# Kernel optimization log

Measured on AMD Instinct MI355X. Metric: run time of the kernel, lower is better.

Reference implementation:

```python
import jax, jax.numpy as jnp
import numpy as np

IN_BIT = 8      # in_bit_width
W_BIT = 2       # weight_bit_width (also output act quantizer bit width)
BN_EPS = 1e-4


def _ste(x, q):
    # straight-through estimator: forward = q, backward = identity w.r.t. x
    return x + jax.lax.stop_gradient(q - x)


def act_quant(x, bit):
    # CommonActQuant: signed int quant, narrow_range=False, power-of-two scale
    # range [-1, 1 - 2^{-(bit-1)}] -> scale = 2^{-(bit-1)}
    s = 2.0 ** (1 - bit)
    n_min = -(2.0 ** (bit - 1))
    n_max = 2.0 ** (bit - 1) - 1.0
    q = jnp.clip(jnp.round(x / s), n_min, n_max) * s
    return _ste(x, q)


def weight_quant(w, bit):
    # CommonWeightQuant: narrow-range signed int quant, unit scaling const
    # scale = 1 / (2^{bit-1} - 1); for bit=2 levels are {-1, 0, 1}
    n = 2.0 ** (bit - 1) - 1.0
    s = 1.0 / n
    q = jnp.clip(jnp.round(w / s), -n, n) * s
    return _ste(w, q)


def setup_inputs() -> dict:
    key = jax.random.key(0)
    k1, k2, k3, k4 = jax.random.split(key, 4)
    B, C, H, W = 32, 256, 32, 32
    x = jax.random.normal(k1, (B, C, H, W), dtype=jnp.float32) * 0.5
    weight = jax.random.normal(k2, (C, C, 3, 3), dtype=jnp.float32) * 0.5
    gamma = jnp.ones((C,), dtype=jnp.float32)
    beta = jnp.zeros((C,), dtype=jnp.float32)
    running_mean = jax.random.normal(k3, (C,), dtype=jnp.float32) * 0.1
    running_var = jax.random.uniform(k4, (C,), dtype=jnp.float32, minval=0.5, maxval=1.5)
    return {"x": x, "weight": weight, "gamma": gamma, "beta": beta,
            "running_mean": running_mean, "running_var": running_var}


def reference(x, weight, gamma, beta, running_mean, running_var):
    # 1) input QuantIdentity (8-bit, [-1, 1-2^-7], power-of-two scale 2^-7)
    xq = act_quant(x, IN_BIT)
    # 2) QuantConv2d 3x3 stride 1 pad 1, no bias, 2-bit weights
    wq = weight_quant(weight, W_BIT)
    y = jax.lax.conv_general_dilated(
        xq, wq, window_strides=(1, 1), padding=((1, 1), (1, 1)),
        dimension_numbers=("NCHW", "OIHW", "NCHW"))
    # 3) BatchNorm2d (inference, eps=1e-4)
    inv = gamma / jnp.sqrt(running_var + BN_EPS)
    y = y * inv[None, :, None, None] + (beta - running_mean * inv)[None, :, None, None]
    # 4) output QuantIdentity at weight_bit_width bits
    return act_quant(y, W_BIT)
```

## Files before the change

### kernel.cpp

```cpp
#include <hip/hip_runtime.h>
#include <hip/hip_bf16.h>
#include <stdint.h>


typedef int i32x4 __attribute__((ext_vector_type(4)));
typedef float f32x4 __attribute__((ext_vector_type(4)));

__device__ __forceinline__ void gload_lds16(const void* g, const void* lds) {
    __builtin_amdgcn_global_load_lds(
        (const __attribute__((address_space(1))) unsigned int*)(uintptr_t)g,
        (__attribute__((address_space(3))) unsigned int*)(uintptr_t)lds,
        16, 0, 0);
}

__global__ __launch_bounds__(256) void quant_kernel(
    const float* __restrict__ x, const float* __restrict__ w,
    signed char* __restrict__ xpad, signed char* __restrict__ wq)
{
    __shared__ signed char tile[32 * 272];
    const int t = threadIdx.x;
    const int blk = blockIdx.x;

    if (blk >= 1088) {
        const int co = blk - 1088;
        signed char* wt = tile;
#pragma unroll
        for (int p = 0; p < 9; ++p) {
            const int idx = p * 256 + t;
            const float v = w[co * 2304 + idx];
            const int ci = idx / 9;
            const int khkw = idx - 9 * ci;
            const float q = fminf(fmaxf(rintf(v), -1.f), 1.f);
            wt[khkw * 256 + ci] = (signed char)(int)q;
        }
        __syncthreads();
        if (t < 144) {
            const int kt = t >> 2, kq = t & 3;
            const uint4 v = *(const uint4*)(wt + t * 16);
            *(uint4*)(wq + ((size_t)((co >> 4) * 36 + kt) << 10) + kq * 256 + (co & 15) * 16) = v;
        }
        return;
    }

    const int b = blk / 34;
    const int hp = blk % 34;
    signed char* rowbase = xpad + (size_t)((b * 34 + hp) * 34) * 256;
    const uint4 z = {0u, 0u, 0u, 0u};
    if (hp == 0 || hp == 33) {
        for (int i = t; i < 544; i += 256) *(uint4*)(rowbase + i * 16) = z;
        return;
    }
    const int h = hp - 1;
    const int ww = t & 31;
    const int cg = (t >> 5) * 4;
#pragma unroll
    for (int p = 0; p < 8; ++p) {
        const int ci = p * 32 + cg;
        unsigned packed = 0;
#pragma unroll
        for (int k = 0; k < 4; ++k) {
            const float v = x[(((size_t)(b * 256 + ci + k)) * 32 + h) * 32 + ww];
            float q = fminf(fmaxf(rintf(__fmul_rn(v, 128.f)), -128.f), 127.f);
            packed |= ((unsigned)(unsigned char)(signed char)(int)q) << (8 * k);
        }
        *(unsigned*)(tile + ww * 272 + ci) = packed;
    }
    __syncthreads();
#pragma unroll
    for (int q = 0; q < 2; ++q) {
        const int wp = q * 16 + (t >> 4);
        const int ci16 = (t & 15) * 16;
        uint4 v = *(const uint4*)(tile + wp * 272 + ci16);
        *(uint4*)(rowbase + (size_t)(wp + 1) * 256 + ci16) = v;
    }
    if (t < 32) {
        const int wp = (t >> 4) * 33;
        *(uint4*)(rowbase + (size_t)wp * 256 + (t & 15) * 16) = z;
    }
}

__global__ __launch_bounds__(256, 3) void conv_gemm_kernel(
    const signed char* __restrict__ xpad, const signed char* __restrict__ wqm,
    const float* __restrict__ gamma, const float* __restrict__ beta,
    const float* __restrict__ mean, const float* __restrict__ var,
    float* __restrict__ out)
{
    __shared__ signed char As[6 * 34 * 256];

    const int tid = threadIdx.x;
    const int wv = tid >> 6;
    const int lane = tid & 63;
    const int l16 = lane & 15;
    const int l4 = lane >> 4;

    const int mt = blockIdx.x >> 1;
    const int n0 = (blockIdx.x & 1) * 128;
    const int b = mt >> 3;
    const int h0 = (mt & 7) * 4;
    const int wave_m = wv & 1;
    const int wave_n = wv >> 1;

    const signed char* xbase = xpad + (size_t)(b * 34 + h0) * 34 * 256;
#pragma unroll
    for (int p = 0; p < 13; ++p) {
        const int i = p * 4 + wv;
        if (i < 51) {
            const int d = i * 64 + lane;
            const int r = d >> 4;
            const int c = d & 15;
            gload_lds16(xbase + r * 256 + ((c ^ (r & 15)) << 4), As + i * 1024);
        }
    }
    __syncthreads();

    int r0[4];
#pragma unroll
    for (int i = 0; i < 4; ++i)
        r0[i] = (wave_m * 2 + (i >> 1)) * 34 + (i & 1) * 16 + l16;

    const signed char* bp[4];
#pragma unroll
    for (int j = 0; j < 4; ++j)
        bp[j] = wqm + (((size_t)((n0 >> 4) + wave_n * 4 + j) * 36) << 10) + lane * 16;

    i32x4 acc[4][4];
#pragma unroll
    for (int i = 0; i < 4; i++)
#pragma unroll
        for (int j = 0; j < 4; j++) acc[i][j] = (i32x4){0, 0, 0, 0};

    i32x4 aP[2][4], bP[2][4];

#define LOAD_B(kt, dst) { _Pragma("unroll") \
                          for (int j = 0; j < 4; ++j) \
                              dst[j] = *(const i32x4*)(bp[j] + (kt) * 1024); }
#define LOAD_A(kt, dst) { const int khkw = (kt) >> 2; \
                          const int kh = khkw / 3; \
                          const int kw = khkw - 3 * kh; \
                          const int roff = kh * 34 + kw; \
                          const int cb = ((kt) & 3) * 4 + l4; \
                          _Pragma("unroll") \
                          for (int i = 0; i < 4; ++i) { \
                              const int r = r0[i] + roff; \
                              dst[i] = *(const i32x4*)(As + r * 256 + ((cb ^ (r & 15)) << 4)); \
                          } }
#define MFMA(af, bf) { _Pragma("unroll") \
                       for (int i = 0; i < 4; ++i) \
                           _Pragma("unroll") \
                           for (int j = 0; j < 4; ++j) \
                               acc[i][j] = __builtin_amdgcn_mfma_i32_16x16x64_i8(af[i], bf[j], acc[i][j], 0, 0, 0); }

    LOAD_B(0, bP[0])
    LOAD_A(0, aP[0])
#pragma unroll
    for (int kt = 0; kt < 36; ++kt) {
        const int cur = kt & 1, nxt = cur ^ 1;
        if (kt + 1 < 36) { LOAD_B(kt + 1, bP[nxt]) LOAD_A(kt + 1, aP[nxt]) }
        MFMA(aP[cur], bP[cur])
    }

#pragma unroll
    for (int j = 0; j < 4; ++j) {
        const int co = n0 + wave_n * 64 + j * 16 + l16;
        const float iv = __fdiv_rn(gamma[co], __fsqrt_rn(__fadd_rn(var[co], 1e-4f)));
        const float bias = __fsub_rn(beta[co], __fmul_rn(mean[co], iv));
#pragma unroll
        for (int i = 0; i < 4; ++i) {
            const int h = h0 + wave_m * 2 + (i >> 1);
            const int w = (i & 1) * 16 + l4 * 4;
            f32x4 v;
#pragma unroll
            for (int r = 0; r < 4; r++) {
                const float y = __fmul_rn((float)acc[i][j][r], 0.0078125f);
                const float t = __fadd_rn(__fmul_rn(y, iv), bias);
                float z = rintf(__fmul_rn(t, 2.f));
                z = fminf(fmaxf(z, -2.f), 1.f);
                v[r] = __fmul_rn(z, 0.5f);
            }
            *(f32x4*)(&out[(((size_t)(b * 256 + co)) * 32 + h) * 32 + w]) = v;
        }
    }
#undef LOAD_B
#undef LOAD_A
#undef MFMA
}

extern "C" void kernel_launch(void* const* d_in, const int* in_sizes, int n_in,
                              void* d_out, int out_size, void* d_ws, size_t ws_size,
                              hipStream_t stream) {
    const float* x      = (const float*)d_in[0];
    const float* weight = (const float*)d_in[1];
    const float* gamma  = (const float*)d_in[2];
    const float* beta   = (const float*)d_in[3];
    const float* rmean  = (const float*)d_in[4];
    const float* rvar   = (const float*)d_in[5];
    float* out = (float*)d_out;

    signed char* wq   = (signed char*)d_ws;
    signed char* xpad = (signed char*)d_ws + (1 << 20);

    quant_kernel<<<1344, 256, 0, stream>>>(x, weight, xpad, wq);
    conv_gemm_kernel<<<512, 256, 0, stream>>>(xpad, wq, gamma, beta, rmean, rvar, out);
}
```

Before: 127.4 us.

## Pack ternary weights as 4-bit nibbles and double waves per conv block

Weights are stored offset by one as 4-bit values, two nibbles per byte, which halves the global bytes read for the B operand. They are expanded back to int8 in registers with a byte-permute lookup before each MFMA. The conv block grows from 4 to 8 waves, each handling one output row instead of two, so per-wave accumulators are halved and more waves share the LDS input tile. The cost is extra VALU unpack work per MFMA and a changed launch configuration.

```diff
diff --git a/kernel.cpp b/kernel.cpp
--- a/kernel.cpp
+++ b/kernel.cpp
@@ -31,13 +31,17 @@
             const int ci = idx / 9;
             const int khkw = idx - 9 * ci;
             const float q = fminf(fmaxf(rintf(v), -1.f), 1.f);
-            wt[khkw * 256 + ci] = (signed char)(int)q;
+            wt[khkw * 256 + ci] = (signed char)(int)(q + 1.f);
         }
         __syncthreads();
         if (t < 144) {
             const int kt = t >> 2, kq = t & 3;
             const uint4 v = *(const uint4*)(wt + t * 16);
-            *(uint4*)(wq + ((size_t)((co >> 4) * 36 + kt) << 10) + kq * 256 + (co & 15) * 16) = v;
+            uint2 o;
+            o.x = v.x | (v.y << 4);
+            o.y = v.z | (v.w << 4);
+            *(uint2*)(wq + ((size_t)((co >> 4) * 18 + (kt >> 1)) << 10)
+                         + ((kq * 16 + (co & 15)) << 4) + (kt & 1) * 8) = o;
         }
         return;
     }
@@ -79,7 +83,7 @@
     }
 }
 
-__global__ __launch_bounds__(256, 3) void conv_gemm_kernel(
+__global__ __launch_bounds__(512, 4) void conv_gemm_kernel(
     const signed char* __restrict__ xpad, const signed char* __restrict__ wqm,
     const float* __restrict__ gamma, const float* __restrict__ beta,
     const float* __restrict__ mean, const float* __restrict__ var,
@@ -97,13 +101,13 @@
     const int n0 = (blockIdx.x & 1) * 128;
     const int b = mt >> 3;
     const int h0 = (mt & 7) * 4;
-    const int wave_m = wv & 1;
-    const int wave_n = wv >> 1;
+    const int wave_m = wv & 3;
+    const int wave_n = wv >> 2;
 
     const signed char* xbase = xpad + (size_t)(b * 34 + h0) * 34 * 256;
 #pragma unroll
-    for (int p = 0; p < 13; ++p) {
-        const int i = p * 4 + wv;
+    for (int p = 0; p < 7; ++p) {
+        const int i = p * 8 + wv;
         if (i < 51) {
             const int d = i * 64 + lane;
             const int r = d >> 4;
@@ -113,50 +117,64 @@
     }
     __syncthreads();
 
-    int r0[4];
-#pragma unroll
-    for (int i = 0; i < 4; ++i)
-        r0[i] = (wave_m * 2 + (i >> 1)) * 34 + (i & 1) * 16 + l16;
-
-    const signed char* bp[4];
+    int r0[2];
+#pragma unroll
+    for (int i = 0; i < 2; ++i)
+        r0[i] = wave_m * 34 + i * 16 + l16;
+
+    const signed char* pbp[4];
 #pragma unroll
     for (int j = 0; j < 4; ++j)
-        bp[j] = wqm + (((size_t)((n0 >> 4) + wave_n * 4 + j) * 36) << 10) + lane * 16;
-
-    i32x4 acc[4][4];
-#pragma unroll
-    for (int i = 0; i < 4; i++)
+        pbp[j] = wqm + (((size_t)(((n0 >> 4) + wave_n * 4 + j) * 18)) << 10) + lane * 16;
+
+    i32x4 acc[2][4];
+#pragma unroll
+    for (int i = 0; i < 2; i++)
 #pragma unroll
         for (int j = 0; j < 4; j++) acc[i][j] = (i32x4){0, 0, 0, 0};
 
-    i32x4 aP[2][4], bP[2][4];
-
-#define LOAD_B(kt, dst) { _Pragma("unroll") \
-                          for (int j = 0; j < 4; ++j) \
-                              dst[j] = *(const i32x4*)(bp[j] + (kt) * 1024); }
+    i32x4 aP[2][2];
+    i32x4 pB[2][4];
+
+    const unsigned LUTC = 0x000100FFu;
+    const unsigned NMSK = 0x0F0F0F0Fu;
+
+#define LOAD_PB(kt2, dst) { _Pragma("unroll") \
+                            for (int j = 0; j < 4; ++j) \
+                                dst[j] = *(const i32x4*)(pbp[j] + (kt2) * 1024); }
 #define LOAD_A(kt, dst) { const int khkw = (kt) >> 2; \
                           const int kh = khkw / 3; \
                           const int kw = khkw - 3 * kh; \
                           const int roff = kh * 34 + kw; \
                           const int cb = ((kt) & 3) * 4 + l4; \
                           _Pragma("unroll") \
-                          for (int i = 0; i < 4; ++i) { \
+                          for (int i = 0; i < 2; ++i) { \
                               const int r = r0[i] + roff; \
                               dst[i] = *(const i32x4*)(As + r * 256 + ((cb ^ (r & 15)) << 4)); \
                           } }
-#define MFMA(af, bf) { _Pragma("unroll") \
-                       for (int i = 0; i < 4; ++i) \
-                           _Pragma("unroll") \
-                           for (int j = 0; j < 4; ++j) \
-                               acc[i][j] = __builtin_amdgcn_mfma_i32_16x16x64_i8(af[i], bf[j], acc[i][j], 0, 0, 0); }
-
-    LOAD_B(0, bP[0])
+#define COMPUTE(af, src, half) { _Pragma("unroll") \
+    for (int j = 0; j < 4; ++j) { \
+        const unsigned d0 = (unsigned)src[j][(half) * 2]; \
+        const unsigned d1 = (unsigned)src[j][(half) * 2 + 1]; \
+        i32x4 bU; \
+        bU[0] = (int)__builtin_amdgcn_perm(0u, LUTC, d0 & NMSK); \
+        bU[1] = (int)__builtin_amdgcn_perm(0u, LUTC, (d0 >> 4) & NMSK); \
+        bU[2] = (int)__builtin_amdgcn_perm(0u, LUTC, d1 & NMSK); \
+        bU[3] = (int)__builtin_amdgcn_perm(0u, LUTC, (d1 >> 4) & NMSK); \
+        acc[0][j] = __builtin_amdgcn_mfma_i32_16x16x64_i8(af[0], bU, acc[0][j], 0, 0, 0); \
+        acc[1][j] = __builtin_amdgcn_mfma_i32_16x16x64_i8(af[1], bU, acc[1][j], 0, 0, 0); \
+    } }
+
+    LOAD_PB(0, pB[0])
     LOAD_A(0, aP[0])
 #pragma unroll
     for (int kt = 0; kt < 36; ++kt) {
         const int cur = kt & 1, nxt = cur ^ 1;
-        if (kt + 1 < 36) { LOAD_B(kt + 1, bP[nxt]) LOAD_A(kt + 1, aP[nxt]) }
-        MFMA(aP[cur], bP[cur])
+        const int kt2 = kt >> 1;
+        const int pcur = kt2 & 1, pnxt = pcur ^ 1;
+        if ((kt & 1) == 0 && kt2 + 1 < 18) { LOAD_PB(kt2 + 1, pB[pnxt]) }
+        if (kt + 1 < 36) { LOAD_A(kt + 1, aP[nxt]) }
+        COMPUTE(aP[cur], pB[pcur], kt & 1)
     }
 
 #pragma unroll
@@ -164,10 +182,10 @@
         const int co = n0 + wave_n * 64 + j * 16 + l16;
         const float iv = __fdiv_rn(gamma[co], __fsqrt_rn(__fadd_rn(var[co], 1e-4f)));
         const float bias = __fsub_rn(beta[co], __fmul_rn(mean[co], iv));
-#pragma unroll
-        for (int i = 0; i < 4; ++i) {
-            const int h = h0 + wave_m * 2 + (i >> 1);
-            const int w = (i & 1) * 16 + l4 * 4;
+        const int h = h0 + wave_m;
+#pragma unroll
+        for (int i = 0; i < 2; ++i) {
+            const int w = i * 16 + l4 * 4;
             f32x4 v;
 #pragma unroll
             for (int r = 0; r < 4; r++) {
@@ -180,9 +198,9 @@
             *(f32x4*)(&out[(((size_t)(b * 256 + co)) * 32 + h) * 32 + w]) = v;
         }
     }
-#undef LOAD_B
+#undef LOAD_PB
 #undef LOAD_A
-#undef MFMA
+#undef COMPUTE
 }
 
 extern "C" void kernel_launch(void* const* d_in, const int* in_sizes, int n_in,
@@ -200,5 +218,5 @@
     signed char* xpad = (signed char*)d_ws + (1 << 20);
 
     quant_kernel<<<1344, 256, 0, stream>>>(x, weight, xpad, wq);
-    conv_gemm_kernel<<<512, 256, 0, stream>>>(xpad, wq, gamma, beta, rmean, rvar, out);
-}
+    conv_gemm_kernel<<<512, 512, 0, stream>>>(xpad, wq, gamma, beta, rmean, rvar, out);
+}
```

After: 121.2 us. 4.8% less time.
